# Kernel tuning notes

Hardware: AMD Instinct MI355X
Metric: run time of the kernel (lower is better)

Reference implementation:

```python
import jax, jax.numpy as jnp
import numpy as np

HID = 128   # hidden_size
EDGE = 16   # edge_size
L = 3       # n_layers
K = 3       # sparse_k
U = 4       # atoms per block (uniform)
NB = 20000  # number of blocks
N = NB * U  # number of atoms
EB = 30000  # number of block-level edges


def _egnn_forward(H, Z, edges, edge_attr,
                  emb_in_w, emb_in_b, emb_out_w, emb_out_b,
                  edge_w1, edge_b1, edge_w2, edge_b2,
                  node_w1, node_b1, node_w2, node_b2,
                  coord_w1, coord_b1, coord_w2):
    # ---- sparse-k atom edges from block edges (uniform U atoms per block) ----
    off = jnp.arange(U)
    src_atoms = edges[0][:, None] * U + off            # [EB, U]
    dst_atoms = edges[1][:, None] * U + off            # [EB, U]
    # squared distances between every src/dst atom pair of each block edge
    d2 = jnp.sum((Z[src_atoms][:, :, None, :] - Z[dst_atoms][:, None, :, :]) ** 2, -1)  # [EB,U,U]
    _, idx = jax.lax.top_k(-d2, K)                     # K nearest dst atoms per src atom
    row = jnp.broadcast_to(src_atoms[:, :, None], (EB, U, K)).reshape(-1)   # [E]
    col = jnp.take_along_axis(jnp.broadcast_to(dst_atoms[:, None, :], (EB, U, U)), idx, axis=2).reshape(-1)
    edge_id = jnp.broadcast_to(jnp.arange(EB)[:, None, None], (EB, U, K)).reshape(-1)
    eattr = edge_attr[edge_id]                         # gather block-edge attr per atom edge [E, EDGE]

    # ---- EGNN (Satorras egnn_clean: SiLU, residual h, mean coord agg) ----
    h = H @ emb_in_w + emb_in_b
    x = Z
    ones = jnp.ones((row.shape[0], 1), Z.dtype)
    cnt = jnp.clip(jax.ops.segment_sum(ones, row, num_segments=N), 1.0)
    for l in range(L):
        diff = x[row] - x[col]                         # [E,3]
        radial = jnp.sum(diff * diff, -1, keepdims=True)
        m = jnp.concatenate([h[row], h[col], radial, eattr], -1)   # [E, 2*HID+1+EDGE]
        m = jax.nn.silu(m @ edge_w1[l] + edge_b1[l])
        m = jax.nn.silu(m @ edge_w2[l] + edge_b2[l])   # edge messages [E, HID]
        # coordinate update (mean aggregation over outgoing edges of row)
        w = jax.nn.silu(m @ coord_w1[l] + coord_b1[l]) @ coord_w2[l]   # [E,1]
        x = x + jax.ops.segment_sum(diff * w, row, num_segments=N) / cnt
        # node update (sum aggregation, residual)
        agg = jax.ops.segment_sum(m, row, num_segments=N)
        hn = jnp.concatenate([h, agg], -1)
        h = h + (jax.nn.silu(hn @ node_w1[l] + node_b1[l]) @ node_w2[l] + node_b2[l])
    h = h @ emb_out_w + emb_out_b
    return h, x


def setup_inputs() -> dict:
    key = jax.random.key(0)
    ks = jax.random.split(key, 16)
    s = 0.05
    p = {}
    p["H"] = jax.random.normal(ks[0], (N, HID), jnp.float32)
    p["Z"] = jax.random.normal(ks[1], (N, 3), jnp.float32) * 3.0
    p["block_id"] = jnp.repeat(jnp.arange(NB, dtype=jnp.int32), U)
    p["batch_id"] = jnp.zeros((N,), jnp.int32)
    p["edges"] = jax.random.randint(ks[2], (2, EB), 0, NB, dtype=jnp.int32)
    p["edge_attr"] = jax.random.normal(ks[3], (EB, EDGE), jnp.float32)
    p["emb_in_w"] = jax.random.normal(ks[4], (HID, HID), jnp.float32) * s
    p["emb_in_b"] = jnp.zeros((HID,), jnp.float32)
    p["emb_out_w"] = jax.random.normal(ks[5], (HID, HID), jnp.float32) * s
    p["emb_out_b"] = jnp.zeros((HID,), jnp.float32)
    p["edge_w1"] = jax.random.normal(ks[6], (L, 2 * HID + 1 + EDGE, HID), jnp.float32) * s
    p["edge_b1"] = jnp.zeros((L, HID), jnp.float32)
    p["edge_w2"] = jax.random.normal(ks[7], (L, HID, HID), jnp.float32) * s
    p["edge_b2"] = jnp.zeros((L, HID), jnp.float32)
    p["node_w1"] = jax.random.normal(ks[8], (L, 2 * HID, HID), jnp.float32) * s
    p["node_b1"] = jnp.zeros((L, HID), jnp.float32)
    p["node_w2"] = jax.random.normal(ks[9], (L, HID, HID), jnp.float32) * s
    p["node_b2"] = jnp.zeros((L, HID), jnp.float32)
    p["coord_w1"] = jax.random.normal(ks[10], (L, HID, HID), jnp.float32) * s
    p["coord_b1"] = jnp.zeros((L, HID), jnp.float32)
    p["coord_w2"] = jax.random.normal(ks[11], (L, HID, 1), jnp.float32) * s
    return p


def reference(H, Z, block_id, batch_id, edges, edge_attr,
              emb_in_w, emb_in_b, emb_out_w, emb_out_b,
              edge_w1, edge_b1, edge_w2, edge_b2,
              node_w1, node_b1, node_w2, node_b2,
              coord_w1, coord_b1, coord_w2):
    # block_id / batch_id are carried for API fidelity; uniform-U block layout is static.
    return _egnn_forward(H, Z, edges, edge_attr,
                         emb_in_w, emb_in_b, emb_out_w, emb_out_b,
                         edge_w1, edge_b1, edge_w2, edge_b2,
                         node_w1, node_b1, node_w2, node_b2,
                         coord_w1, coord_b1, coord_w2)
```

## Files before the change

### kernel.cpp

```cpp
#include <hip/hip_runtime.h>
#include <math.h>

#define HIDC 128
#define EDGEF 16
#define LAY 3
#define KNN 3
#define UU 4
#define NBLK 20000
#define NATOM (NBLK*UU)
#define EBK 30000
#define EALL (EBK*UU*KNN)
#define NGRP (EBK*UU)

#define W1F_L 36864
#define W2F_L 16384
#define NW1F_L 32768

typedef __attribute__((ext_vector_type(8))) short bf16x8;
typedef __attribute__((ext_vector_type(4))) float f32x4;

__device__ __forceinline__ float silu_f(float v) {
    return __fdividef(v, 1.0f + __expf(-v));
}

__device__ __forceinline__ unsigned short f2bf(float f) {
    union { float f; unsigned int u; } v; v.f = f;
    unsigned int r = v.u + 0x7FFFu + ((v.u >> 16) & 1u);
    return (unsigned short)(r >> 16);
}

__device__ __forceinline__ float bf2f(unsigned short h) {
    union { unsigned int u; float f; } t; t.u = ((unsigned int)h) << 16;
    return t.f;
}

__device__ __forceinline__ void split2(float v, short& hi, short& lo) {
    unsigned short h = f2bf(v);
    hi = (short)h;
    lo = (short)f2bf(v - bf2f(h));
}

__device__ __forceinline__ void csplit(float v, unsigned short& hi, unsigned short& lo) {
    unsigned int hu = __float_as_uint(v) & 0xffff0000u;
    hi = (unsigned short)(hu >> 16);
    lo = f2bf(v - __uint_as_float(hu));
}

__device__ __forceinline__ unsigned int packhl(float v) {
    unsigned int hu = __float_as_uint(v) & 0xffff0000u;
    return hu | (unsigned int)f2bf(v - __uint_as_float(hu));
}

__device__ __forceinline__ float unpackf(unsigned int u) {
    return bf2f((unsigned short)(u >> 16)) + bf2f((unsigned short)(u & 0xffffu));
}

__device__ __forceinline__ void unpack8(uint4 v0, uint4 v1, bf16x8& ah, bf16x8& al) {
    unsigned int uu[8] = {v0.x, v0.y, v0.z, v0.w, v1.x, v1.y, v1.z, v1.w};
    #pragma unroll
    for (int q = 0; q < 8; q++) {
        ah[q] = (short)(unsigned short)(uu[q] >> 16);
        al[q] = (short)(unsigned short)(uu[q] & 0xffffu);
    }
}

__device__ __forceinline__ void stage16(const unsigned short* gsrc, unsigned short* ldst) {
    __builtin_amdgcn_global_load_lds(
        (const __attribute__((address_space(1))) unsigned int*)(const void*)gsrc,
        (__attribute__((address_space(3))) unsigned int*)(void*)ldst,
        16, 0, 0);
}


__global__ void k_count(const int* __restrict__ edges, int* __restrict__ degB) {
    int e = blockIdx.x * 256 + threadIdx.x;
    if (e < EBK) atomicAdd(&degB[edges[e]], 1);
}

__global__ void k_scan(const int* __restrict__ degB, int* __restrict__ offB) {
    __shared__ int s[1024];
    __shared__ int carry;
    if (threadIdx.x == 0) carry = 0;
    __syncthreads();
    for (int base = 0; base < NBLK; base += 1024) {
        int i = base + threadIdx.x;
        int v = (i < NBLK) ? degB[i] : 0;
        s[threadIdx.x] = v;
        __syncthreads();
        for (int d = 1; d < 1024; d <<= 1) {
            int t = (threadIdx.x >= d) ? s[threadIdx.x - d] : 0;
            __syncthreads();
            s[threadIdx.x] += t;
            __syncthreads();
        }
        if (i < NBLK) offB[i] = carry + s[threadIdx.x] - v;
        int tot = s[1023];
        __syncthreads();
        if (threadIdx.x == 0) carry += tot;
        __syncthreads();
    }
    if (threadIdx.x == 0) offB[NBLK] = carry;
}

__global__ void k_fill(const int* __restrict__ edges, const int* __restrict__ offB,
                       int* __restrict__ cursor, int* __restrict__ listE) {
    int e = blockIdx.x * 256 + threadIdx.x;
    if (e < EBK) {
        int b = edges[e];
        int p = atomicAdd(&cursor[b], 1);
        listE[offB[b] + p] = e;
    }
}

__global__ void k_topk(const int* __restrict__ edges, const float* __restrict__ Z,
                       int* __restrict__ colIdx) {
    int t = blockIdx.x * 256 + threadIdx.x;
    if (t >= EBK * UU) return;
    int e = t >> 2, u = t & 3;
    int b0 = edges[e], b1 = edges[EBK + e];
    int s = b0 * UU + u;
    float zs0 = Z[s*3+0], zs1 = Z[s*3+1], zs2 = Z[s*3+2];
    float d2[UU];
    #pragma unroll
    for (int v = 0; v < UU; v++) {
        int d = b1 * UU + v;
        float a0 = __fsub_rn(zs0, Z[d*3+0]);
        float a1 = __fsub_rn(zs1, Z[d*3+1]);
        float a2 = __fsub_rn(zs2, Z[d*3+2]);
        float p0 = __fmul_rn(a0, a0);
        float p1 = __fmul_rn(a1, a1);
        float p2 = __fmul_rn(a2, a2);
        d2[v] = __fadd_rn(__fadd_rn(p0, p1), p2);
    }
    bool used[UU] = {false, false, false, false};
    #pragma unroll
    for (int k = 0; k < KNN; k++) {
        int best = -1;
        float bd = INFINITY;
        #pragma unroll
        for (int v = 0; v < UU; v++) {
            if (!used[v] && d2[v] < bd) { bd = d2[v]; best = v; }
        }
        used[best] = true;
        colIdx[t * KNN + k] = b1 * UU + best;
    }
}


__global__ void k_wfrag(const float* __restrict__ ew1, const float* __restrict__ ew2,
                        const float* __restrict__ cw1,
                        const float* __restrict__ nw1, const float* __restrict__ nw2,
                        unsigned short* __restrict__ w1f_hi, unsigned short* __restrict__ w1f_lo,
                        unsigned short* __restrict__ w2f_hi, unsigned short* __restrict__ w2f_lo,
                        unsigned short* __restrict__ c1f_hi, unsigned short* __restrict__ c1f_lo,
                        unsigned short* __restrict__ n1f_hi, unsigned short* __restrict__ n1f_lo,
                        unsigned short* __restrict__ n2f_hi, unsigned short* __restrict__ n2f_lo) {
    int i = blockIdx.x * 256 + threadIdx.x;
    float v = 0.f;
    unsigned short* dh = nullptr;
    unsigned short* dl = nullptr;
    int di = 0;
    if (i < 3 * W1F_L) {
        int l = i / W1F_L, rem = i % W1F_L;
        int chunk = rem >> 9, lane = (rem >> 3) & 63, t = rem & 7;
        int kb = chunk >> 3, j = chunk & 7;
        int k = kb*32 + (lane >> 4)*8 + t, n = j*16 + (lane & 15);
        v = (k < 273) ? ew1[(size_t)l*273*128 + (size_t)k*128 + n] : 0.f;
        dh = w1f_hi; dl = w1f_lo; di = i;
    } else {
        int i2 = i - 3 * W1F_L;
        if (i2 < 3 * W2F_L) {
            int l = i2 / W2F_L, rem = i2 % W2F_L;
            int chunk = rem >> 9, lane = (rem >> 3) & 63, t = rem & 7;
            int kb = chunk >> 3, j = chunk & 7;
            int k = kb*32 + (lane >> 4)*8 + t, n = j*16 + (lane & 15);
            v = ew2[(size_t)l*128*128 + (size_t)k*128 + n];
            dh = w2f_hi; dl = w2f_lo; di = i2;
        } else {
            int i3 = i2 - 3 * W2F_L;
            if (i3 < 3 * W2F_L) {
                int l = i3 / W2F_L, rem = i3 % W2F_L;
                int chunk = rem >> 9, lane = (rem >> 3) & 63, t = rem & 7;
                int kb = chunk >> 3, j = chunk & 7;
                int k = kb*32 + (lane >> 4)*8 + t, n = j*16 + (lane & 15);
                v = cw1[(size_t)l*128*128 + (size_t)k*128 + n];
                dh = c1f_hi; dl = c1f_lo; di = i3;
            } else {
                int i4 = i3 - 3 * W2F_L;
                if (i4 < 3 * NW1F_L) {
                    int l = i4 / NW1F_L, rem = i4 % NW1F_L;
                    int chunk = rem >> 9, lane = (rem >> 3) & 63, t = rem & 7;
                    int kb = chunk >> 3, j = chunk & 7;
                    int k = kb*32 + (lane >> 4)*8 + t, n = j*16 + (lane & 15);
                    v = nw1[(size_t)l*256*128 + (size_t)k*128 + n];
                    dh = n1f_hi; dl = n1f_lo; di = i4;
                } else {
                    int i5 = i4 - 3 * NW1F_L;
                    if (i5 >= 3 * W2F_L) return;
                    int l = i5 / W2F_L, rem = i5 % W2F_L;
                    int chunk = rem >> 9, lane = (rem >> 3) & 63, t = rem & 7;
                    int kb = chunk >> 3, j = chunk & 7;
                    int k = kb*32 + (lane >> 4)*8 + t, n = j*16 + (lane & 15);
                    v = nw2[(size_t)l*128*128 + (size_t)k*128 + n];
                    dh = n2f_hi; dl = n2f_lo; di = i5;
                }
            }
        }
    }
    short hi, lo;
    split2(v, hi, lo);
    dh[di] = (unsigned short)hi;
    dl[di] = (unsigned short)lo;
}


__global__ __launch_bounds__(256, 4) void k_edge_shared(
    const unsigned int* __restrict__ hp,
    const float* __restrict__ x,
    const float* __restrict__ eattr,
    const int* __restrict__ edges0,
    const int* __restrict__ colIdx,
    const unsigned short* __restrict__ w1f_hi, const unsigned short* __restrict__ w1f_lo,
    const unsigned short* __restrict__ w2f_hi, const unsigned short* __restrict__ w2f_lo,
    const unsigned short* __restrict__ c1f_hi, const unsigned short* __restrict__ c1f_lo,
    const float* __restrict__ eb1,
    const float* __restrict__ eb2,
    const float* __restrict__ cb1,
    const float* __restrict__ cw2v,
    unsigned short* __restrict__ msum,
    float* __restrict__ xsum)
{
    __shared__ unsigned short wbufH[4096], wbufL[4096];
    __shared__ unsigned short C1[4][16 * 128];
    __shared__ float diffS[4][48];

    const int tid = threadIdx.x;
    const int wid = tid >> 6, l = tid & 63;
    const int g = l >> 4, er = l & 15;
    const int u = er >> 2, kk = er & 3;
    const int kkc = (kk < 3) ? kk : 2;
    const int e = blockIdx.x * 4 + wid;

    const int bs = edges0[e];
    const int srcA = bs * 4 + u;
    const int colA = colIdx[(e * 4 + u) * 3 + kkc];
    float rad = 0.f;
    if (g == 0) {
        float dx = x[srcA*3+0] - x[colA*3+0];
        float dy = x[srcA*3+1] - x[colA*3+1];
        float dz = x[srcA*3+2] - x[colA*3+2];
        rad = dx*dx + dy*dy + dz*dz;
        diffS[wid][er*3+0] = dx; diffS[wid][er*3+1] = dy; diffS[wid][er*3+2] = dz;
    }

    const int goff = wid * 512 + l * 8;
    unsigned short* lb0H = wbufH + wid * 512;
    unsigned short* lb1H = wbufH + 2048 + wid * 512;
    unsigned short* lb0L = wbufL + wid * 512;
    unsigned short* lb1L = wbufL + 2048 + wid * 512;

    {
        f32x4 acc[8];
        #pragma unroll
        for (int jj = 0; jj < 8; jj++) acc[jj] = (f32x4){0.f, 0.f, 0.f, 0.f};

        #pragma unroll 1
        for (int kb = 0; kb < 9; kb++) {
            __syncthreads();
            stage16(w1f_hi + (kb << 12) + goff,        lb0H);
            stage16(w1f_hi + (kb << 12) + 2048 + goff, lb1H);
            stage16(w1f_lo + (kb << 12) + goff,        lb0L);
            stage16(w1f_lo + (kb << 12) + 2048 + goff, lb1L);
            bf16x8 ah, al;
            if (kb < 8) {
                const unsigned int* src = (kb < 4) ? (hp + (size_t)srcA * 128 + kb * 32 + g * 8)
                                                   : (hp + (size_t)colA * 128 + (kb - 4) * 32 + g * 8);
                uint4 v0 = *(const uint4*)src;
                uint4 v1 = *((const uint4*)src + 1);
                unpack8(v0, v1, ah, al);
            } else {
                float tv[8];
                #pragma unroll
                for (int q = 0; q < 8; q++) tv[q] = 0.f;
                if (g == 0) {
                    tv[0] = rad;
                    #pragma unroll
                    for (int q = 1; q < 8; q++) tv[q] = eattr[(size_t)e*16 + (q-1)];
                } else if (g == 1) {
                    #pragma unroll
                    for (int q = 0; q < 8; q++) tv[q] = eattr[(size_t)e*16 + 7 + q];
                } else if (g == 2) {
                    tv[0] = eattr[(size_t)e*16 + 15];
                }
                #pragma unroll
                for (int q = 0; q < 8; q++) { unsigned short hh, ll; csplit(tv[q], hh, ll); ah[q] = (short)hh; al[q] = (short)ll; }
            }
            __syncthreads();
            __builtin_amdgcn_s_setprio(1);
            #pragma unroll
            for (int jj = 0; jj < 8; jj++) {
                const int off = (jj << 9) + (l << 3);
                bf16x8 wh = *(const bf16x8*)&wbufH[off];
                bf16x8 wl = *(const bf16x8*)&wbufL[off];
                acc[jj] = __builtin_amdgcn_mfma_f32_16x16x32_bf16(ah, wh, acc[jj], 0, 0, 0);
                acc[jj] = __builtin_amdgcn_mfma_f32_16x16x32_bf16(al, wh, acc[jj], 0, 0, 0);
                acc[jj] = __builtin_amdgcn_mfma_f32_16x16x32_bf16(ah, wl, acc[jj], 0, 0, 0);
            }
            __builtin_amdgcn_s_setprio(0);
        }
        #pragma unroll
        for (int jj = 0; jj < 8; jj++) {
            const int n = jj * 16 + er;
            const float bv = eb1[n];
            #pragma unroll
            for (int reg = 0; reg < 4; reg++) {
                const int row = g * 4 + reg;
                float v = silu_f(acc[jj][reg] + bv);
                C1[wid][row * 128 + (n ^ ((row & 7) << 3))] = f2bf(v);
            }
        }
    }

    {
        f32x4 acc[8];
        #pragma unroll
        for (int jj = 0; jj < 8; jj++) acc[jj] = (f32x4){0.f, 0.f, 0.f, 0.f};

        #pragma unroll 1
        for (int kb = 0; kb < 4; kb++) {
            __syncthreads();
            stage16(w2f_hi + (kb << 12) + goff,        lb0H);
            stage16(w2f_hi + (kb << 12) + 2048 + goff, lb1H);
            stage16(w2f_lo + (kb << 12) + goff,        lb0L);
            stage16(w2f_lo + (kb << 12) + 2048 + goff, lb1L);
            const int aoff = er * 128 + ((kb * 32 + g * 8) ^ ((er & 7) << 3));
            bf16x8 a2 = *(const bf16x8*)&C1[wid][aoff];
            __syncthreads();
            __builtin_amdgcn_s_setprio(1);
            #pragma unroll
            for (int jj = 0; jj < 8; jj++) {
                const int off = (jj << 9) + (l << 3);
                bf16x8 wh = *(const bf16x8*)&wbufH[off];
                bf16x8 wl = *(const bf16x8*)&wbufL[off];
                acc[jj] = __builtin_amdgcn_mfma_f32_16x16x32_bf16(a2, wh, acc[jj], 0, 0, 0);
                acc[jj] = __builtin_amdgcn_mfma_f32_16x16x32_bf16(a2, wl, acc[jj], 0, 0, 0);
            }
            __builtin_amdgcn_s_setprio(0);
        }
        #pragma unroll
        for (int jj = 0; jj < 8; jj++) {
            const int n = jj * 16 + er;
            const float bv = eb2[n];
            float ms = 0.f;
            #pragma unroll
            for (int reg = 0; reg < 4; reg++) {
                const int row = g * 4 + reg;
                float v = silu_f(acc[jj][reg] + bv);
                if (reg < 3) ms += v;
                C1[wid][row * 128 + (n ^ ((row & 7) << 3))] = f2bf(v);
            }
            msum[(size_t)(e * 4 + g) * 128 + n] = f2bf(ms);
        }
    }

    {
        f32x4 acc[8];
        #pragma unroll
        for (int jj = 0; jj < 8; jj++) acc[jj] = (f32x4){0.f, 0.f, 0.f, 0.f};

        #pragma unroll 1
        for (int kb = 0; kb < 4; kb++) {
            __syncthreads();
            stage16(c1f_hi + (kb << 12) + goff,        lb0H);
            stage16(c1f_hi + (kb << 12) + 2048 + goff, lb1H);
            stage16(c1f_lo + (kb << 12) + goff,        lb0L);
            stage16(c1f_lo + (kb << 12) + 2048 + goff, lb1L);
            const int aoff = er * 128 + ((kb * 32 + g * 8) ^ ((er & 7) << 3));
            bf16x8 a3 = *(const bf16x8*)&C1[wid][aoff];
            __syncthreads();
            __builtin_amdgcn_s_setprio(1);
            #pragma unroll
            for (int jj = 0; jj < 8; jj++) {
                const int off = (jj << 9) + (l << 3);
                bf16x8 wh = *(const bf16x8*)&wbufH[off];
                bf16x8 wl = *(const bf16x8*)&wbufL[off];
                acc[jj] = __builtin_amdgcn_mfma_f32_16x16x32_bf16(a3, wh, acc[jj], 0, 0, 0);
                acc[jj] = __builtin_amdgcn_mfma_f32_16x16x32_bf16(a3, wl, acc[jj], 0, 0, 0);
            }
            __builtin_amdgcn_s_setprio(0);
        }
        float p[4] = {0.f, 0.f, 0.f, 0.f};
        #pragma unroll
        for (int jj = 0; jj < 8; jj++) {
            const int n = jj * 16 + er;
            const float cb = cb1[n], cw = cw2v[n];
            #pragma unroll
            for (int reg = 0; reg < 4; reg++)
                p[reg] += silu_f(acc[jj][reg] + cb) * cw;
        }
        #pragma unroll
        for (int d = 1; d < 16; d <<= 1) {
            #pragma unroll
            for (int reg = 0; reg < 4; reg++)
                p[reg] += __shfl_xor(p[reg], d);
        }
        if (er < 3) {
            float xs = 0.f;
            #pragma unroll
            for (int reg = 0; reg < 3; reg++)
                xs += diffS[wid][(g * 4 + reg) * 3 + er] * p[reg];
            xsum[(size_t)(e * 4 + g) * 3 + er] = xs;
        }
    }
}


__global__ void k_xupd(const float* __restrict__ xcur, const float* __restrict__ xsum,
                       const int* __restrict__ offB, const int* __restrict__ listE,
                       float* __restrict__ xnext)
{
    int i = blockIdx.x * 256 + threadIdx.x;
    if (i >= NATOM * 3) return;
    int a = i / 3, d = i - a * 3;
    int b = a >> 2, u = a & 3;
    int o0 = offB[b], o1 = offB[b + 1];
    float xs = 0.f;
    for (int pos = o0; pos < o1; pos++) {
        int e = listE[pos];
        xs += xsum[(size_t)(e * 4 + u) * 3 + d];
    }
    int deg = o1 - o0;
    xnext[i] = xcur[i] + ((deg > 0) ? xs / (3.0f * (float)deg) : 0.f);
}


__global__ __launch_bounds__(256, 4) void k_node(
    unsigned int* __restrict__ hp,
    const unsigned short* __restrict__ msum,
    const int* __restrict__ offB,
    const int* __restrict__ listE,
    const unsigned short* __restrict__ n1f_hi, const unsigned short* __restrict__ n1f_lo,
    const unsigned short* __restrict__ n2f_hi, const unsigned short* __restrict__ n2f_lo,
    const float* __restrict__ nb1,
    const float* __restrict__ nb2)
{
    __shared__ unsigned short wbufH[4096], wbufL[4096];
    __shared__ unsigned short hid[4][16 * 128];

    const int tid = threadIdx.x;
    const int wid = tid >> 6, l = tid & 63;
    const int g = l >> 4, er = l & 15;
    const int a0 = blockIdx.x * 64 + wid * 16;
    const int a = a0 + er;
    const int b = a >> 2, u = a & 3;
    const int o0 = offB[b], o1 = offB[b + 1];

    const int goff = wid * 512 + l * 8;
    unsigned short* lb0H = wbufH + wid * 512;
    unsigned short* lb1H = wbufH + 2048 + wid * 512;
    unsigned short* lb0L = wbufL + wid * 512;
    unsigned short* lb1L = wbufL + 2048 + wid * 512;

    {
        f32x4 acc[8];
        #pragma unroll
        for (int jj = 0; jj < 8; jj++) acc[jj] = (f32x4){0.f, 0.f, 0.f, 0.f};

        #pragma unroll 1
        for (int kb = 0; kb < 8; kb++) {
            __syncthreads();
            stage16(n1f_hi + (kb << 12) + goff,        lb0H);
            stage16(n1f_hi + (kb << 12) + 2048 + goff, lb1H);
            stage16(n1f_lo + (kb << 12) + goff,        lb0L);
            stage16(n1f_lo + (kb << 12) + 2048 + goff, lb1L);
            bf16x8 ah, al;
            if (kb < 4) {
                const unsigned int* src = hp + (size_t)a * 128 + kb * 32 + g * 8;
                uint4 v0 = *(const uint4*)src;
                uint4 v1 = *((const uint4*)src + 1);
                unpack8(v0, v1, ah, al);
            } else {
                float s[8];
                #pragma unroll
                for (int q = 0; q < 8; q++) s[q] = 0.f;
                for (int pos = o0; pos < o1; pos++) {
                    const int e = listE[pos];
                    bf16x8 mv = *(const bf16x8*)(msum + (size_t)(e * 4 + u) * 128 + (kb - 4) * 32 + g * 8);
                    #pragma unroll
                    for (int q = 0; q < 8; q++) s[q] += bf2f((unsigned short)mv[q]);
                }
                #pragma unroll
                for (int q = 0; q < 8; q++) { unsigned short hh, ll; csplit(s[q], hh, ll); ah[q] = (short)hh; al[q] = (short)ll; }
            }
            __syncthreads();
            __builtin_amdgcn_s_setprio(1);
            #pragma unroll
            for (int jj = 0; jj < 8; jj++) {
                const int off = (jj << 9) + (l << 3);
                bf16x8 wh = *(const bf16x8*)&wbufH[off];
                bf16x8 wl = *(const bf16x8*)&wbufL[off];
                acc[jj] = __builtin_amdgcn_mfma_f32_16x16x32_bf16(ah, wh, acc[jj], 0, 0, 0);
                acc[jj] = __builtin_amdgcn_mfma_f32_16x16x32_bf16(al, wh, acc[jj], 0, 0, 0);
                acc[jj] = __builtin_amdgcn_mfma_f32_16x16x32_bf16(ah, wl, acc[jj], 0, 0, 0);
            }
            __builtin_amdgcn_s_setprio(0);
        }
        #pragma unroll
        for (int jj = 0; jj < 8; jj++) {
            const int n = jj * 16 + er;
            const float bv = nb1[n];
            #pragma unroll
            for (int reg = 0; reg < 4; reg++) {
                const int row = g * 4 + reg;
                float v = silu_f(acc[jj][reg] + bv);
                hid[wid][row * 128 + (n ^ ((row & 7) << 3))] = f2bf(v);
            }
        }
    }

    {
        f32x4 acc[8];
        #pragma unroll
        for (int jj = 0; jj < 8; jj++) acc[jj] = (f32x4){0.f, 0.f, 0.f, 0.f};

        #pragma unroll 1
        for (int kb = 0; kb < 4; kb++) {
            __syncthreads();
            stage16(n2f_hi + (kb << 12) + goff,        lb0H);
            stage16(n2f_hi + (kb << 12) + 2048 + goff, lb1H);
            stage16(n2f_lo + (kb << 12) + goff,        lb0L);
            stage16(n2f_lo + (kb << 12) + 2048 + goff, lb1L);
            const int aoff = er * 128 + ((kb * 32 + g * 8) ^ ((er & 7) << 3));
            bf16x8 ab = *(const bf16x8*)&hid[wid][aoff];
            __syncthreads();
            __builtin_amdgcn_s_setprio(1);
            #pragma unroll
            for (int jj = 0; jj < 8; jj++) {
                const int off = (jj << 9) + (l << 3);
                bf16x8 wh = *(const bf16x8*)&wbufH[off];
                bf16x8 wl = *(const bf16x8*)&wbufL[off];
                acc[jj] = __builtin_amdgcn_mfma_f32_16x16x32_bf16(ab, wh, acc[jj], 0, 0, 0);
                acc[jj] = __builtin_amdgcn_mfma_f32_16x16x32_bf16(ab, wl, acc[jj], 0, 0, 0);
            }
            __builtin_amdgcn_s_setprio(0);
        }
        #pragma unroll
        for (int jj = 0; jj < 8; jj++) {
            const int n = jj * 16 + er;
            const float bv = nb2[n];
            #pragma unroll
            for (int reg = 0; reg < 4; reg++) {
                const int row = g * 4 + reg;
                const size_t idx = (size_t)(a0 + row) * 128 + n;
                float v = acc[jj][reg] + bv + unpackf(hp[idx]);
                hp[idx] = packhl(v);
            }
        }
    }
}


template<int KT, bool PACKIN, bool PACKOUT>
__global__ __launch_bounds__(128) void k_gemm(
    const float* __restrict__ A0,
    const float* __restrict__ W, const float* __restrict__ bias,
    float* __restrict__ C, int M)
{
    __shared__ float At[KT][32];
    __shared__ float Bs[32][128];
    const int tid = threadIdx.x;
    const int tile0 = blockIdx.x * 32;
    const int r = tid >> 2, part = tid & 3;
    const int gr = tile0 + r;

    if (gr < M) {
        #pragma unroll
        for (int j = 0; j < 8; j++) {
            int c = part * 32 + j * 4;
            float f0, f1, f2, f3;
            if (PACKIN) {
                const unsigned int* ap = (const unsigned int*)A0 + (size_t)gr * 128 + c;
                uint4 v = *(const uint4*)ap;
                f0 = unpackf(v.x); f1 = unpackf(v.y); f2 = unpackf(v.z); f3 = unpackf(v.w);
            } else {
                float4 v = *(const float4*)(A0 + (size_t)gr * 128 + c);
                f0 = v.x; f1 = v.y; f2 = v.z; f3 = v.w;
            }
            At[c][r] = f0; At[c+1][r] = f1; At[c+2][r] = f2; At[c+3][r] = f3;
        }
    } else {
        #pragma unroll
        for (int j = 0; j < 8; j++) {
            int c = part * 32 + j * 4;
            At[c][r] = 0.f; At[c+1][r] = 0.f; At[c+2][r] = 0.f; At[c+3][r] = 0.f;
        }
    }

    float acc[4][8];
    #pragma unroll
    for (int i = 0; i < 4; i++)
        #pragma unroll
        for (int j = 0; j < 8; j++) acc[i][j] = 0.f;

    const int tx = tid & 15, ty = tid >> 4;

    for (int kb = 0; kb < KT / 32; kb++) {
        __syncthreads();
        #pragma unroll
        for (int j = 0; j < 8; j++) {
            int li = j * 512 + tid * 4;
            int kk = li >> 7, c = li & 127;
            float4 v = *(const float4*)(W + (size_t)(kb * 32 + kk) * 128 + c);
            *(float4*)&Bs[kk][c] = v;
        }
        __syncthreads();
        #pragma unroll 8
        for (int kk = 0; kk < 32; kk++) {
            float4 a  = *(const float4*)&At[kb * 32 + kk][ty * 4];
            float4 b0 = *(const float4*)&Bs[kk][tx * 8];
            float4 b1 = *(const float4*)&Bs[kk][tx * 8 + 4];
            float av[4] = {a.x, a.y, a.z, a.w};
            float bv[8] = {b0.x, b0.y, b0.z, b0.w, b1.x, b1.y, b1.z, b1.w};
            #pragma unroll
            for (int i = 0; i < 4; i++)
                #pragma unroll
                for (int j = 0; j < 8; j++)
                    acc[i][j] = fmaf(av[i], bv[j], acc[i][j]);
        }
    }

    #pragma unroll
    for (int i = 0; i < 4; i++) {
        int grr = tile0 + ty * 4 + i;
        if (grr >= M) continue;
        #pragma unroll
        for (int j = 0; j < 8; j++) {
            int c = tx * 8 + j;
            float v = acc[i][j] + bias[c];
            if (PACKOUT) ((unsigned int*)C)[(size_t)grr * 128 + c] = packhl(v);
            else         C[(size_t)grr * 128 + c] = v;
        }
    }
}


extern "C" void kernel_launch(void* const* d_in, const int* in_sizes, int n_in,
                              void* d_out, int out_size, void* d_ws, size_t ws_size,
                              hipStream_t stream) {
    const float* H        = (const float*)d_in[0];
    const float* Z        = (const float*)d_in[1];
    const int*   edges    = (const int*)  d_in[4];
    const float* eattr    = (const float*)d_in[5];
    const float* emb_in_w = (const float*)d_in[6];
    const float* emb_in_b = (const float*)d_in[7];
    const float* emb_out_w= (const float*)d_in[8];
    const float* emb_out_b= (const float*)d_in[9];
    const float* edge_w1  = (const float*)d_in[10];
    const float* edge_b1  = (const float*)d_in[11];
    const float* edge_w2  = (const float*)d_in[12];
    const float* edge_b2  = (const float*)d_in[13];
    const float* node_w1  = (const float*)d_in[14];
    const float* node_b1  = (const float*)d_in[15];
    const float* node_w2  = (const float*)d_in[16];
    const float* node_b2  = (const float*)d_in[17];
    const float* coord_w1 = (const float*)d_in[18];
    const float* coord_b1 = (const float*)d_in[19];
    const float* coord_w2 = (const float*)d_in[20];

    float* out  = (float*)d_out;
    float* hbuf = out;
    unsigned int* hp = (unsigned int*)hbuf;
    float* xout = out + (size_t)NATOM * 128;

    char* w = (char*)d_ws;
    unsigned short* msum = (unsigned short*)w;  w += (size_t)NGRP * 128 * 2;
    float* xsum = (float*)w;           w += (size_t)NGRP * 3 * 4;
    float* xA  = (float*)w;            w += (size_t)NATOM * 3 * 4;
    float* xB  = (float*)w;            w += (size_t)NATOM * 3 * 4;
    unsigned short* w1f_hi = (unsigned short*)w;  w += (size_t)3 * W1F_L * 2;
    unsigned short* w1f_lo = (unsigned short*)w;  w += (size_t)3 * W1F_L * 2;
    unsigned short* w2f_hi = (unsigned short*)w;  w += (size_t)3 * W2F_L * 2;
    unsigned short* w2f_lo = (unsigned short*)w;  w += (size_t)3 * W2F_L * 2;
    unsigned short* c1f_hi = (unsigned short*)w;  w += (size_t)3 * W2F_L * 2;
    unsigned short* c1f_lo = (unsigned short*)w;  w += (size_t)3 * W2F_L * 2;
    unsigned short* n1f_hi = (unsigned short*)w;  w += (size_t)3 * NW1F_L * 2;
    unsigned short* n1f_lo = (unsigned short*)w;  w += (size_t)3 * NW1F_L * 2;
    unsigned short* n2f_hi = (unsigned short*)w;  w += (size_t)3 * W2F_L * 2;
    unsigned short* n2f_lo = (unsigned short*)w;  w += (size_t)3 * W2F_L * 2;
    int* colIdx = (int*)w;             w += (size_t)EALL * 4;
    int* degB   = (int*)w;             w += (size_t)NBLK * 4;
    int* cursor = (int*)w;             w += (size_t)NBLK * 4;
    int* listE  = (int*)w;             w += (size_t)EBK * 4;
    int* offB   = (int*)w;             w += (size_t)(NBLK + 1) * 4;

    hipMemsetAsync(degB,   0, NBLK * sizeof(int), stream);
    hipMemsetAsync(cursor, 0, NBLK * sizeof(int), stream);

    k_count<<<(EBK + 255) / 256, 256, 0, stream>>>(edges, degB);
    k_scan <<<1, 1024, 0, stream>>>(degB, offB);
    k_fill <<<(EBK + 255) / 256, 256, 0, stream>>>(edges, offB, cursor, listE);
    k_topk <<<(EBK * UU + 255) / 256, 256, 0, stream>>>(edges, Z, colIdx);

    {
        int total = 3 * W1F_L + 3 * W2F_L + 3 * W2F_L + 3 * NW1F_L + 3 * W2F_L;
        k_wfrag<<<(total + 255) / 256, 256, 0, stream>>>(
            edge_w1, edge_w2, coord_w1, node_w1, node_w2,
            w1f_hi, w1f_lo, w2f_hi, w2f_lo, c1f_hi, c1f_lo,
            n1f_hi, n1f_lo, n2f_hi, n2f_lo);
    }

    k_gemm<128, false, true><<<NATOM / 32, 128, 0, stream>>>(
        H, emb_in_w, emb_in_b, (float*)hp, NATOM);

    const float* xcur = Z;
    for (int l = 0; l < LAY; l++) {
        float* xnext = (l == 0) ? xA : (l == 1) ? xB : xout;

        k_edge_shared<<<EBK / 4, 256, 0, stream>>>(
            hp, xcur, eattr, edges, colIdx,
            w1f_hi + (size_t)l * W1F_L, w1f_lo + (size_t)l * W1F_L,
            w2f_hi + (size_t)l * W2F_L, w2f_lo + (size_t)l * W2F_L,
            c1f_hi + (size_t)l * W2F_L, c1f_lo + (size_t)l * W2F_L,
            edge_b1 + l * 128, edge_b2 + l * 128, coord_b1 + l * 128, coord_w2 + l * 128,
            msum, xsum);

        k_xupd<<<(NATOM * 3 + 255) / 256, 256, 0, stream>>>(xcur, xsum, offB, listE, xnext);

        k_node<<<NATOM / 64, 256, 0, stream>>>(
            hp, msum, offB, listE,
            n1f_hi + (size_t)l * NW1F_L, n1f_lo + (size_t)l * NW1F_L,
            n2f_hi + (size_t)l * W2F_L, n2f_lo + (size_t)l * W2F_L,
            node_b1 + l * 128, node_b2 + l * 128);

        xcur = xnext;
    }

    k_gemm<128, true, false><<<NATOM / 32, 128, 0, stream>>>(
        hbuf, emb_out_w, emb_out_b, hbuf, NATOM);
}
```

Before: 1.000 ms.

## Pack edge rows densely across 12-wave workgroups to remove padded MFMA rows

The old edge kernel gave each wave one block edge with 16 MFMA rows, of which only 12 were real atom edges (the fourth neighbour slot was a duplicate). The new kernel puts 16 block edges (192 rows) in a 768-thread workgroup, so every 16-row MFMA tile is filled with real edges and the padded work disappears. Weight staging is now done by 4 of the 12 waves and shared by all of them. The per-atom message and coordinate reductions move to cross-wave LDS passes after extra barriers. The cost is more LDS per workgroup, more threads waiting at each barrier, and possibly lower occupancy.

```diff
diff --git a/kernel.cpp b/kernel.cpp
--- a/kernel.cpp
+++ b/kernel.cpp
@@ -15,6 +15,10 @@
 #define W1F_L 36864
 #define W2F_L 16384
 #define NW1F_L 32768
+
+#define E_WG 16
+#define ROWS_WG (E_WG*12)
+#define WAVES_WG 12
 
 typedef __attribute__((ext_vector_type(8))) short bf16x8;
 typedef __attribute__((ext_vector_type(4))) float f32x4;
@@ -214,7 +218,7 @@
 }
 
 
-__global__ __launch_bounds__(256, 4) void k_edge_shared(
+__global__ __launch_bounds__(768, 6) void k_edge_flat(
     const unsigned int* __restrict__ hp,
     const float* __restrict__ x,
     const float* __restrict__ eattr,
@@ -231,26 +235,32 @@
     float* __restrict__ xsum)
 {
     __shared__ unsigned short wbufH[4096], wbufL[4096];
-    __shared__ unsigned short C1[4][16 * 128];
-    __shared__ float diffS[4][48];
+    __shared__ unsigned short Mlds[ROWS_WG * 128];
+    __shared__ float diffLDS[ROWS_WG][3];
+    __shared__ float pLDS[ROWS_WG];
 
     const int tid = threadIdx.x;
     const int wid = tid >> 6, l = tid & 63;
     const int g = l >> 4, er = l & 15;
-    const int u = er >> 2, kk = er & 3;
-    const int kkc = (kk < 3) ? kk : 2;
-    const int e = blockIdx.x * 4 + wid;
-
+    const int e_base = blockIdx.x * E_WG;
+    const int r0 = wid * 16;
+
+    const int row_g = r0 + er;
+    const int e_loc = row_g / 12;
+    const int rr = row_g - e_loc * 12;
+    const int u = rr / 3;
+    const int kk = rr - u * 3;
+    const int e = e_base + e_loc;
     const int bs = edges0[e];
     const int srcA = bs * 4 + u;
-    const int colA = colIdx[(e * 4 + u) * 3 + kkc];
+    const int colA = colIdx[(e * 4 + u) * 3 + kk];
     float rad = 0.f;
     if (g == 0) {
         float dx = x[srcA*3+0] - x[colA*3+0];
         float dy = x[srcA*3+1] - x[colA*3+1];
         float dz = x[srcA*3+2] - x[colA*3+2];
         rad = dx*dx + dy*dy + dz*dz;
-        diffS[wid][er*3+0] = dx; diffS[wid][er*3+1] = dy; diffS[wid][er*3+2] = dz;
+        diffLDS[row_g][0] = dx; diffLDS[row_g][1] = dy; diffLDS[row_g][2] = dz;
     }
 
     const int goff = wid * 512 + l * 8;
@@ -267,10 +277,12 @@
         #pragma unroll 1
         for (int kb = 0; kb < 9; kb++) {
             __syncthreads();
-            stage16(w1f_hi + (kb << 12) + goff,        lb0H);
-            stage16(w1f_hi + (kb << 12) + 2048 + goff, lb1H);
-            stage16(w1f_lo + (kb << 12) + goff,        lb0L);
-            stage16(w1f_lo + (kb << 12) + 2048 + goff, lb1L);
+            if (wid < 4) {
+                stage16(w1f_hi + (kb << 12) + goff,        lb0H);
+                stage16(w1f_hi + (kb << 12) + 2048 + goff, lb1H);
+                stage16(w1f_lo + (kb << 12) + goff,        lb0L);
+                stage16(w1f_lo + (kb << 12) + 2048 + goff, lb1L);
+            }
             bf16x8 ah, al;
             if (kb < 8) {
                 const unsigned int* src = (kb < 4) ? (hp + (size_t)srcA * 128 + kb * 32 + g * 8)
@@ -314,9 +326,9 @@
             const float bv = eb1[n];
             #pragma unroll
             for (int reg = 0; reg < 4; reg++) {
-                const int row = g * 4 + reg;
+                const int row = r0 + g * 4 + reg;
                 float v = silu_f(acc[jj][reg] + bv);
-                C1[wid][row * 128 + (n ^ ((row & 7) << 3))] = f2bf(v);
+                Mlds[row * 128 + (n ^ ((row & 7) << 3))] = f2bf(v);
             }
         }
     }
@@ -329,12 +341,14 @@
         #pragma unroll 1
         for (int kb = 0; kb < 4; kb++) {
             __syncthreads();
-            stage16(w2f_hi + (kb << 12) + goff,        lb0H);
-            stage16(w2f_hi + (kb << 12) + 2048 + goff, lb1H);
-            stage16(w2f_lo + (kb << 12) + goff,        lb0L);
-            stage16(w2f_lo + (kb << 12) + 2048 + goff, lb1L);
-            const int aoff = er * 128 + ((kb * 32 + g * 8) ^ ((er & 7) << 3));
-            bf16x8 a2 = *(const bf16x8*)&C1[wid][aoff];
+            if (wid < 4) {
+                stage16(w2f_hi + (kb << 12) + goff,        lb0H);
+                stage16(w2f_hi + (kb << 12) + 2048 + goff, lb1H);
+                stage16(w2f_lo + (kb << 12) + goff,        lb0L);
+                stage16(w2f_lo + (kb << 12) + 2048 + goff, lb1L);
+            }
+            const int aoff = row_g * 128 + ((kb * 32 + g * 8) ^ ((row_g & 7) << 3));
+            bf16x8 a2 = *(const bf16x8*)&Mlds[aoff];
             __syncthreads();
             __builtin_amdgcn_s_setprio(1);
             #pragma unroll
@@ -351,15 +365,29 @@
         for (int jj = 0; jj < 8; jj++) {
             const int n = jj * 16 + er;
             const float bv = eb2[n];
+            #pragma unroll
+            for (int reg = 0; reg < 4; reg++) {
+                const int row = r0 + g * 4 + reg;
+                float v = silu_f(acc[jj][reg] + bv);
+                Mlds[row * 128 + (n ^ ((row & 7) << 3))] = f2bf(v);
+            }
+        }
+    }
+    __syncthreads();
+
+    {
+        const int col = tid & 127;
+        const int gslot = tid >> 7;
+        for (int gi = gslot; gi < E_WG * 4; gi += 6) {
+            const int el = gi >> 2, uu2 = gi & 3;
+            const int base = el * 12 + uu2 * 3;
             float ms = 0.f;
             #pragma unroll
-            for (int reg = 0; reg < 4; reg++) {
-                const int row = g * 4 + reg;
-                float v = silu_f(acc[jj][reg] + bv);
-                if (reg < 3) ms += v;
-                C1[wid][row * 128 + (n ^ ((row & 7) << 3))] = f2bf(v);
-            }
-            msum[(size_t)(e * 4 + g) * 128 + n] = f2bf(ms);
+            for (int k3 = 0; k3 < 3; k3++) {
+                const int row = base + k3;
+                ms += bf2f(Mlds[row * 128 + (col ^ ((row & 7) << 3))]);
+            }
+            msum[(size_t)((e_base + el) * 4 + uu2) * 128 + col] = f2bf(ms);
         }
     }
 
@@ -371,12 +399,14 @@
         #pragma unroll 1
         for (int kb = 0; kb < 4; kb++) {
             __syncthreads();
-            stage16(c1f_hi + (kb << 12) + goff,        lb0H);
-            stage16(c1f_hi + (kb << 12) + 2048 + goff, lb1H);
-            stage16(c1f_lo + (kb << 12) + goff,        lb0L);
-            stage16(c1f_lo + (kb << 12) + 2048 + goff, lb1L);
-            const int aoff = er * 128 + ((kb * 32 + g * 8) ^ ((er & 7) << 3));
-            bf16x8 a3 = *(const bf16x8*)&C1[wid][aoff];
+            if (wid < 4) {
+                stage16(c1f_hi + (kb << 12) + goff,        lb0H);
+                stage16(c1f_hi + (kb << 12) + 2048 + goff, lb1H);
+                stage16(c1f_lo + (kb << 12) + goff,        lb0L);
+                stage16(c1f_lo + (kb << 12) + 2048 + goff, lb1L);
+            }
+            const int aoff = row_g * 128 + ((kb * 32 + g * 8) ^ ((row_g & 7) << 3));
+            bf16x8 a3 = *(const bf16x8*)&Mlds[aoff];
             __syncthreads();
             __builtin_amdgcn_s_setprio(1);
             #pragma unroll
@@ -404,13 +434,23 @@
             for (int reg = 0; reg < 4; reg++)
                 p[reg] += __shfl_xor(p[reg], d);
         }
-        if (er < 3) {
-            float xs = 0.f;
-            #pragma unroll
-            for (int reg = 0; reg < 3; reg++)
-                xs += diffS[wid][(g * 4 + reg) * 3 + er] * p[reg];
-            xsum[(size_t)(e * 4 + g) * 3 + er] = xs;
-        }
+        if (er == 0) {
+            #pragma unroll
+            for (int reg = 0; reg < 4; reg++)
+                pLDS[r0 + g * 4 + reg] = p[reg];
+        }
+    }
+    __syncthreads();
+
+    if (tid < E_WG * 4 * 3) {
+        const int gi = tid / 3, c = tid - gi * 3;
+        const int el = gi >> 2, uu2 = gi & 3;
+        const int base = el * 12 + uu2 * 3;
+        float xs = 0.f;
+        #pragma unroll
+        for (int k3 = 0; k3 < 3; k3++)
+            xs += diffLDS[base + k3][c] * pLDS[base + k3];
+        xsum[(size_t)((e_base + el) * 4 + uu2) * 3 + c] = xs;
     }
 }
 
@@ -716,7 +756,7 @@
     for (int l = 0; l < LAY; l++) {
         float* xnext = (l == 0) ? xA : (l == 1) ? xB : xout;
 
-        k_edge_shared<<<EBK / 4, 256, 0, stream>>>(
+        k_edge_flat<<<EBK / E_WG, 768, 0, stream>>>(
             hp, xcur, eattr, edges, colIdx,
             w1f_hi + (size_t)l * W1F_L, w1f_lo + (size_t)l * W1F_L,
             w2f_hi + (size_t)l * W2F_L, w2f_lo + (size_t)l * W2F_L,
```

Result: faster. 895.7 us (-10.4%).
